# Performance work log

Measured on AMD Instinct MI355X. Metric: run time of the kernel, lower is better.

Reference implementation:

```python
import jax, jax.numpy as jnp
from jax import lax
import numpy as np

EPS = 1e-5
STRIDE = 4
K_NEIGHBORS = 16


def setup_inputs() -> dict:
    key = jax.random.key(0)
    ks = jax.random.split(key, 4)
    B, N, Cin, Cout = 16, 4096, 64, 128
    p1 = jax.random.normal(ks[0], (B, N, 3), dtype=jnp.float32)
    x1 = jax.random.normal(ks[1], (B, Cin, N), dtype=jnp.float32)
    w1 = jax.random.normal(ks[2], (Cout, Cin + 3), dtype=jnp.float32) * 0.05
    w2 = jax.random.normal(ks[3], (Cout, Cout), dtype=jnp.float32) * 0.05
    g1 = jnp.ones((Cout,), jnp.float32)
    b1 = jnp.zeros((Cout,), jnp.float32)
    g2 = jnp.ones((Cout,), jnp.float32)
    b2 = jnp.zeros((Cout,), jnp.float32)
    return {"p1": p1, "x1": x1, "w1": w1, "g1": g1, "b1": b1,
            "w2": w2, "g2": g2, "b2": b2}


def farthest_point_sampling(p, npoint):
    # p: [B, N, 3] -> centroids [B, npoint] (deterministic start at index 0)
    B, N, _ = p.shape
    gather_pt = jax.vmap(lambda pts, f: pts[f])  # [B,N,3],[B] -> [B,3]

    def step(carry, _):
        dist, farthest = carry
        centroid = gather_pt(p, farthest)                     # [B, 3]
        d = jnp.sum((p - centroid[:, None, :]) ** 2, -1)      # [B, N]
        dist = jnp.minimum(dist, d)
        new_far = jnp.argmax(dist, axis=-1).astype(jnp.int32)
        return (dist, new_far), farthest

    init = (jnp.full((B, N), 1e10, dtype=p.dtype), jnp.zeros((B,), jnp.int32))
    _, idxs = lax.scan(step, init, None, length=npoint)       # [npoint, B]
    return idxs.T                                             # [B, npoint]


def knn_point(k, xyz, new_xyz):
    # squared distances via gram trick; exclude all-zero points like the original
    n1 = jnp.sum(xyz ** 2, -1)                                # [B, N]
    n2 = jnp.sum(new_xyz ** 2, -1)                            # [B, M]
    d2 = n2[:, :, None] + n1[:, None, :] - 2.0 * jnp.einsum('bmc,bnc->bmn', new_xyz, xyz)
    zero_mask = jnp.all(xyz == 0, axis=-1)                    # [B, N]
    d2 = jnp.where(zero_mask[:, None, :], jnp.inf, d2)
    _, idx = lax.top_k(-d2, k)                                # smallest-k -> [B, M, k]
    return idx


def _bn_relu(h, g, b):
    # BatchNorm2d (training-mode batch stats, biased var) over (B, M, k) per channel
    m = jnp.mean(h, axis=(0, 1, 2), keepdims=True)
    v = jnp.mean((h - m) ** 2, axis=(0, 1, 2), keepdims=True)
    return jax.nn.relu(g * (h - m) * lax.rsqrt(v + EPS) + b)


def reference(p1, x1, w1, g1, b1, w2, g2, b2):
    B, N, _ = p1.shape
    M = max(1, N // STRIDE)
    k = K_NEIGHBORS

    idx = farthest_point_sampling(p1, M)                      # [B, M]
    gather2 = jax.vmap(lambda pts, i: pts[i])
    p2 = gather2(p1, idx)                                     # [B, M, 3]

    idx_knn = knn_point(k, p1, p2)                            # [B, M, k]
    grouped_p1 = gather2(p1, idx_knn)                         # [B, M, k, 3]
    xt = jnp.transpose(x1, (0, 2, 1))                         # [B, N, Cin]
    grouped_x1 = gather2(xt, idx_knn)                         # [B, M, k, Cin]

    rel = grouped_p1 - p2[:, :, None, :]                      # [B, M, k, 3]
    feats = jnp.concatenate([rel, grouped_x1], axis=-1)       # [B, M, k, 3+Cin]

    h = _bn_relu(jnp.einsum('bmkc,oc->bmko', feats, w1), g1, b1)
    h = _bn_relu(jnp.einsum('bmkc,oc->bmko', h, w2), g2, b2)
    new_features = jnp.max(h, axis=2)                         # maxpool over k -> [B, M, Cout]
    return p2, jnp.transpose(new_features, (0, 2, 1))         # ([B,M,3], [B,Cout,M])
```

## Files before the change

kernel.cpp:

```cpp
#include <hip/hip_runtime.h>
#include <hip/hip_bf16.h>
#include <hip/hip_cooperative_groups.h>
#include <cstdint>

namespace cg = cooperative_groups;

#define BB 16
#define NN 4096
#define MM 1024
#define KNB 16
#define CIN 64
#define COUT 128
#define RTOT (BB*MM*KNB)
#define AP1 104
#define AP2 136

typedef __attribute__((ext_vector_type(8))) short short8v;
typedef __attribute__((ext_vector_type(4))) float floatx4;
typedef __attribute__((ext_vector_type(2))) float f32x2;
typedef __attribute__((ext_vector_type(2))) unsigned int uint2v;

__device__ __forceinline__ float bflo(uint32_t u){ return __uint_as_float(u << 16); }
__device__ __forceinline__ float bfhi(uint32_t u){ return __uint_as_float(u & 0xffff0000u); }
__device__ __forceinline__ uint32_t f2bf_pk(float a, float b){
  uint32_t ua = __float_as_uint(a), ub = __float_as_uint(b);
  ua += 0x7fffu + ((ua >> 16) & 1u);
  ub += 0x7fffu + ((ub >> 16) & 1u);
  return (ua >> 16) | (ub & 0xffff0000u);
}
__device__ __forceinline__ uint16_t f2bf1(float a){
  uint32_t u = __float_as_uint(a);
  u += 0x7fffu + ((u >> 16) & 1u);
  return (uint16_t)(u >> 16);
}
template<int CTRL>
__device__ __forceinline__ float dpp_f(float v){
  return __int_as_float(__builtin_amdgcn_update_dpp(__float_as_int(v), __float_as_int(v), CTRL, 0xf, 0xf, false));
}
__device__ __forceinline__ float plmax16(float v){
#if __has_builtin(__builtin_amdgcn_permlane16_swap)
  uint2v r = __builtin_amdgcn_permlane16_swap(__float_as_uint(v), __float_as_uint(v), false, false);
  return fmaxf(__uint_as_float(r[0]), __uint_as_float(r[1]));
#else
  return fmaxf(v, __int_as_float(__builtin_amdgcn_ds_swizzle(__float_as_int(v), 0x401F)));
#endif
}
__device__ __forceinline__ float plmax32(float v){
#if __has_builtin(__builtin_amdgcn_permlane32_swap)
  uint2v r = __builtin_amdgcn_permlane32_swap(__float_as_uint(v), __float_as_uint(v), false, false);
  return fmaxf(__uint_as_float(r[0]), __uint_as_float(r[1]));
#else
  return fmaxf(v, __shfl_xor(v, 32));
#endif
}

struct FpsS { float4 pcv[NN]; float4 sel[MM]; unsigned long long candk[2][4]; };
struct TrS  { float t[64][65]; };
struct ConsS{ uint16_t Bh1[128*AP1]; uint16_t AhD[128*AP2];
              int winq[8*16]; float ssum[128]; float ssq[128]; };
union PreU  { FpsS fps; TrS tr; ConsS cons; };

__global__ __launch_bounds__(512, 2) void k_pre2(
    const float* __restrict__ p1, const float* __restrict__ x1,
    const float* __restrict__ w1,
    float* __restrict__ outp2, float* __restrict__ p2w,
    float4* __restrict__ p1n, uint16_t* __restrict__ xtb, float* __restrict__ Sz,
    uint16_t* __restrict__ h1, float* __restrict__ S1,
    int* __restrict__ prog, int* __restrict__ prep_done)
{
  __shared__ PreU u;
  const int blk = blockIdx.x, tid = threadIdx.x;
  const int lane = tid & 63, wid = tid >> 6;

  if (blk < 16){
    int b = blk;
    const float* pb = p1 + (size_t)b*NN*3;
    {
      float4 f[6];
      const float4* src = (const float4*)(pb + tid*24);
      #pragma unroll
      for (int j=0;j<6;j++) f[j] = src[j];
      const float* fa = (const float*)f;
      #pragma unroll
      for (int j=0;j<8;j++)
        u.fps.pcv[tid*8 + j] = make_float4(fa[3*j], fa[3*j+1], fa[3*j+2], 0.f);
    }
    __syncthreads();
    float4 c00 = u.fps.pcv[0];
    float cx = c00.x, cy = c00.y, cz = c00.z;
    if (tid==64) u.fps.sel[0] = make_float4(cx, cy, cz, 0.f);

    f32x2 px2[8] = {}, py2[8] = {}, pz2[8] = {}, ds2[8] = {};
    const int g0 = tid*16;
    if (wid < 4){
      #pragma unroll
      for (int j=0;j<8;j++){
        float4 a = u.fps.pcv[g0 + 2*j];
        float4 bq = u.fps.pcv[g0 + 2*j + 1];
        px2[j][0]=a.x; px2[j][1]=bq.x;
        py2[j][0]=a.y; py2[j][1]=bq.y;
        pz2[j][0]=a.z; pz2[j][1]=bq.z;
        ds2[j][0]=1e10f; ds2[j][1]=1e10f;
      }
    }

    for (int i=1;i<MM;i++){
      if (wid < 4){
        {
          #pragma clang fp contract(off)
          f32x2 cx2; cx2[0]=cx; cx2[1]=cx;
          f32x2 cy2; cy2[0]=cy; cy2[1]=cy;
          f32x2 cz2; cz2[0]=cz; cz2[1]=cz;
          #pragma unroll
          for (int j=0;j<8;j++){
            f32x2 dx = px2[j] - cx2;
            f32x2 dy = py2[j] - cy2;
            f32x2 dz = pz2[j] - cz2;
            f32x2 d  = dx*dx + dy*dy + dz*dz;
            ds2[j] = __builtin_elementwise_min(ds2[j], d);
          }
        }
        f32x2 t0 = __builtin_elementwise_max(ds2[0], ds2[1]);
        f32x2 t1 = __builtin_elementwise_max(ds2[2], ds2[3]);
        f32x2 t2 = __builtin_elementwise_max(ds2[4], ds2[5]);
        f32x2 t3 = __builtin_elementwise_max(ds2[6], ds2[7]);
        f32x2 u0 = __builtin_elementwise_max(t0, t1);
        f32x2 u1 = __builtin_elementwise_max(t2, t3);
        f32x2 vv = __builtin_elementwise_max(u0, u1);
        float lm = fmaxf(vv[0], vv[1]);
        int li = g0 + 15;
        #pragma unroll
        for (int j=14;j>=0;j--){
          float ev = ds2[j>>1][j & 1];
          li = (ev == lm) ? (g0 + j) : li;
        }
        float wm = lm;
        wm = fmaxf(wm, dpp_f<0xB1>(wm));
        wm = fmaxf(wm, dpp_f<0x4E>(wm));
        wm = fmaxf(wm, dpp_f<0x124>(wm));
        wm = fmaxf(wm, dpp_f<0x128>(wm));
        wm = plmax16(wm);
        wm = plmax32(wm);
        unsigned long long bmask = __ballot(lm == wm);
        int fl = __ffsll(bmask) - 1;
        int wi = __builtin_amdgcn_readlane(li, fl);
        if (lane == 0)
          u.fps.candk[i&1][wid] = (((unsigned long long)(unsigned)__float_as_uint(wm)) << 32)
                                   | (unsigned)(0xFFFFu ^ (unsigned)wi);
      }
      __syncthreads();
      if (wid < 4){
        const unsigned long long* cd = u.fps.candk[i&1];
        unsigned long long cq0=cd[0], cq1=cd[1], cq2=cd[2], cq3=cd[3];
        unsigned long long a0 = cq0>cq1?cq0:cq1, a1 = cq2>cq3?cq2:cq3;
        unsigned long long mb = a0>a1?a0:a1;
        int midx = (int)(0xFFFFu ^ (unsigned)(mb & 0xFFFFull));
        float4 cv = u.fps.pcv[midx];
        cx = cv.x; cy = cv.y; cz = cv.z;
        if (tid==64) u.fps.sel[i] = make_float4(cx, cy, cz, 0.f);
      } else if (wid == 4 && (i & 63) == 0){
        int e = i - 64 + lane;
        float4 s = u.fps.sel[e];
        float n2 = __fadd_rn(__fadd_rn(__fmul_rn(s.x,s.x),__fmul_rn(s.y,s.y)),__fmul_rn(s.z,s.z));
        *(float4*)(p2w + ((size_t)b*MM + e)*4) = make_float4(s.x, s.y, s.z, n2);
        if (lane == 0)
          __hip_atomic_store(&prog[b*16], i, __ATOMIC_RELEASE, __HIP_MEMORY_SCOPE_AGENT);
      }
    }
    __syncthreads();
    if (wid == 4){
      int e = 960 + lane;
      float4 s = u.fps.sel[e];
      float n2 = __fadd_rn(__fadd_rn(__fmul_rn(s.x,s.x),__fmul_rn(s.y,s.y)),__fmul_rn(s.z,s.z));
      *(float4*)(p2w + ((size_t)b*MM + e)*4) = make_float4(s.x, s.y, s.z, n2);
      if (lane == 0)
        __hip_atomic_store(&prog[b*16], MM, __ATOMIC_RELEASE, __HIP_MEMORY_SCOPE_AGENT);
    }
    for (int e = tid; e < MM; e += 512){
      float4 s = u.fps.sel[e];
      float* o = outp2 + ((size_t)b*MM + e)*3;
      o[0]=s.x; o[1]=s.y; o[2]=s.z;
    }
  } else {
    for (int i = (blk-16)*512 + tid; i < 16384; i += 240*512) Sz[i] = 0.f;
    for (int i = (blk-16)*512 + tid; i < BB*NN; i += 240*512){
      float x = p1[(size_t)i*3+0], y = p1[(size_t)i*3+1], z = p1[(size_t)i*3+2];
      float n = __fadd_rn(__fadd_rn(__fmul_rn(x,x),__fmul_rn(y,y)),__fmul_rn(z,z));
      p1n[i] = make_float4(x,y,z,n);
    }
    for (int tile = blk-16; tile < 1024; tile += 240){
      int b = tile >> 6, n0 = (tile & 63)*64;
      __syncthreads();
      int c = tid >> 3, q = tid & 7;
      const float* src = x1 + ((size_t)(b*64 + c))*NN + n0 + q*8;
      float4 f0 = *(const float4*)src, f1 = *(const float4*)(src+4);
      u.tr.t[c][q*8+0]=f0.x; u.tr.t[c][q*8+1]=f0.y; u.tr.t[c][q*8+2]=f0.z; u.tr.t[c][q*8+3]=f0.w;
      u.tr.t[c][q*8+4]=f1.x; u.tr.t[c][q*8+5]=f1.y; u.tr.t[c][q*8+6]=f1.z; u.tr.t[c][q*8+7]=f1.w;
      __syncthreads();
      int n = tid >> 3;
      uint32_t* dst = (uint32_t*)(xtb + ((size_t)(b*NN + n0 + n))*64 + q*8);
      #pragma unroll
      for (int j=0;j<4;j++)
        dst[j] = f2bf_pk(u.tr.t[q*8+2*j][n], u.tr.t[q*8+2*j+1][n]);
    }
    __threadfence();
    __syncthreads();
    if (tid == 0) atomicAdd(prep_done, 1);
    for (int e = tid; e < 128*96; e += 512){
      int o = e / 96, k = e - o*96;
      float v = (k < 64) ? w1[o*67 + 3 + k] : ((k < 67) ? w1[o*67 + (k-64)] : 0.f);
      u.cons.Bh1[o*AP1 + k] = f2bf1(v);
    }
    if (tid < 128){ u.cons.ssum[tid]=0.f; u.cons.ssq[tid]=0.f; }
    __syncthreads();
    {
      int pv = 0, sp = 0;
      if (lane == 0) pv = __hip_atomic_load(prep_done, __ATOMIC_ACQUIRE, __HIP_MEMORY_SCOPE_AGENT);
      pv = __shfl(pv, 0);
      while (pv < 240 && sp < (1<<16)){
        __builtin_amdgcn_s_sleep(64);
        if (lane == 0) pv = __hip_atomic_load(prep_done, __ATOMIC_ACQUIRE, __HIP_MEMORY_SCOPE_AGENT);
        pv = __shfl(pv, 0); sp++;
      }
    }
    int ml = lane & 15, quad = lane >> 4, seg = lane >> 4;
    int gw = (blk-16)*8 + wid;
    for (int qi = gw; qi < BB*MM; qi += 1920){
      int b = qi & 15, m = qi >> 4;
      int q2 = b*MM + m;
      {
        int pv = 0, sp = 0;
        if (lane == 0) pv = __hip_atomic_load(&prog[b*16], __ATOMIC_ACQUIRE, __HIP_MEMORY_SCOPE_AGENT);
        pv = __shfl(pv, 0);
        while (pv <= m && sp < (1<<16)){
          __builtin_amdgcn_s_sleep(64);
          if (lane == 0) pv = __hip_atomic_load(&prog[b*16], __ATOMIC_ACQUIRE, __HIP_MEMORY_SCOPE_AGENT);
          pv = __shfl(pv, 0); sp++;
        }
      }
      const float4 qv = *(const float4*)(p2w + (size_t)q2*4);
      const float4* pbn = p1n + (size_t)b*NN;
      float bd[16]; int bi[16];
      #pragma unroll
      for (int s=0;s<16;s++){ bd[s] = 1e30f; bi[s] = 0; }
      float wv = 1e30f; int wslot = 0;

      #define KPROC(T, PV) { \
        float dot = fmaf(qv.z, (PV).z, fmaf(qv.y, (PV).y, __fmul_rn(qv.x, (PV).x))); \
        float d2 = __fsub_rn(__fadd_rn(qv.w, (PV).w), __fmul_rn(2.0f, dot)); \
        if (d2 < wv){ \
          int c = (T)*64 + lane; \
          _Pragma("unroll") \
          for (int s=0;s<16;s++) if (s==wslot){ bd[s]=d2; bi[s]=c; } \
          wv = bd[0]; wslot = 0; \
          _Pragma("unroll") \
          for (int s=1;s<16;s++) if (bd[s] > wv){ wv = bd[s]; wslot = s; } \
        } }

      float4 cur = pbn[lane];
      for (int t=0;t<63;t++){
        float4 nx = pbn[(t+1)*64 + lane];
        KPROC(t, cur);
        cur = nx;
      }
      KPROC(63, cur);
      #undef KPROC

      float lv = bd[0]; int ls = 0;
      #pragma unroll
      for (int s=1;s<16;s++) if (bd[s] < lv){ lv = bd[s]; ls = s; }
      for (int r=0;r<16;r++){
        float rv = lv; int rl = lane;
        #pragma unroll
        for (int off=32; off>=1; off>>=1){
          float ov = __shfl_xor(rv, off); int ol = __shfl_xor(rl, off);
          if (ov < rv || (ov == rv && ol < rl)){ rv = ov; rl = ol; }
        }
        if (lane == rl){
          int idx = 0;
          #pragma unroll
          for (int s=0;s<16;s++) if (s==ls) idx = bi[s];
          u.cons.winq[wid*16 + r] = idx;
          #pragma unroll
          for (int s=0;s<16;s++) if (s==ls) bd[s] = 1e30f;
          lv = bd[0]; ls = 0;
          #pragma unroll
          for (int s=1;s<16;s++) if (bd[s] < lv){ lv = bd[s]; ls = s; }
        }
      }
      int n = u.cons.winq[wid*16 + ml];
      {
        const uint4* s4 = (const uint4*)(xtb + ((size_t)(b*NN + n))*64 + seg*16);
        uint4* d4 = (uint4*)(u.cons.AhD + (wid*16 + ml)*AP2 + seg*16);
        d4[0] = s4[0]; d4[1] = s4[1];
        if (seg == 0){
          const float* pp = p1 + ((size_t)(b*NN + n))*3;
          float rx = __fsub_rn(pp[0], qv.x);
          float ry = __fsub_rn(pp[1], qv.y);
          float rz = __fsub_rn(pp[2], qv.z);
          uint4* dr = (uint4*)(u.cons.AhD + (wid*16 + ml)*AP2 + 64);
          dr[0] = make_uint4(f2bf_pk(rx, ry), f2bf_pk(rz, 0.f), 0u, 0u);
          dr[1] = make_uint4(0u,0u,0u,0u);
          dr[2] = make_uint4(0u,0u,0u,0u);
          dr[3] = make_uint4(0u,0u,0u,0u);
        }
      }
      short8v af[3];
      #pragma unroll
      for (int kc=0;kc<3;kc++)
        af[kc] = *(const short8v*)(u.cons.AhD + (wid*16 + ml)*AP2 + kc*32 + quad*8);
      floatx4 acc[8];
      #pragma unroll
      for (int ct=0;ct<8;ct++) acc[ct] = (floatx4){0.f,0.f,0.f,0.f};
      #pragma unroll
      for (int ct=0;ct<8;ct++){
        #pragma unroll
        for (int kc=0;kc<3;kc++){
          short8v bf = *(const short8v*)(u.cons.Bh1 + (ct*16+ml)*AP1 + kc*32 + quad*8);
          acc[ct] = __builtin_amdgcn_mfma_f32_16x16x32_bf16(af[kc], bf, acc[ct], 0, 0, 0);
        }
      }
      float csum[8], csq[8];
      #pragma unroll
      for (int ct=0;ct<8;ct++){
        float a0=acc[ct][0], a1=acc[ct][1], a2=acc[ct][2], a3=acc[ct][3];
        float s = (a0+a1)+(a2+a3);
        float qq2 = (a0*a0+a1*a1)+(a2*a2+a3*a3);
        s += __shfl_xor(s,16);  s += __shfl_xor(s,32);
        qq2 += __shfl_xor(qq2,16); qq2 += __shfl_xor(qq2,32);
        csum[ct]=s; csq[ct]=qq2;
        #pragma unroll
        for (int r=0;r<4;r++)
          u.cons.AhD[(wid*16 + quad*4 + r)*AP2 + ct*16 + ml] = f2bf1(acc[ct][r]);
      }
      #pragma unroll
      for (int jj=0;jj<2;jj++){
        int ct = quad*2 + jj, col = ct*16 + ml;
        atomicAdd(&u.cons.ssum[col], csum[ct]);
        atomicAdd(&u.cons.ssq[col],  csq[ct]);
      }
      {
        const uint4* s4 = (const uint4*)(u.cons.AhD + (wid*16 + ml)*AP2 + seg*32);
        uint4* dst = (uint4*)(h1 + ((size_t)q2*16 + ml)*128 + seg*32);
        dst[0]=s4[0]; dst[1]=s4[1]; dst[2]=s4[2]; dst[3]=s4[3];
      }
    }
    __syncthreads();
    int cp = (blk & 31)*256;
    if (tid < 128){ atomicAdd(&S1[cp+tid], u.cons.ssum[tid]); atomicAdd(&S1[cp+128+tid], u.cons.ssq[tid]); }
  }
}

__global__ __launch_bounds__(256) void k_gemm2(const __hip_bfloat16* __restrict__ h1,
                                               const float* __restrict__ w2,
                                               const float* __restrict__ g1v, const float* __restrict__ b1v,
                                               const float* __restrict__ S1, float* __restrict__ S2,
                                               float* __restrict__ hmax, float* __restrict__ hmin){
  __shared__ __hip_bfloat16 Ah[64*AP2];
  __shared__ __hip_bfloat16 Bh[128*AP2];
  __shared__ float scb[128], shb[128], ssum[128], ssq[128];
  int tid = threadIdx.x;
  if (tid < 128){
    float s=0.f, q=0.f;
    for (int c=0;c<32;c++){ s += S1[c*256+tid]; q += S1[c*256+128+tid]; }
    float inv = 1.0f / (float)RTOT;
    float mean = s * inv;
    float var  = q * inv - mean*mean;
    float rs = 1.0f / sqrtf(var + 1e-5f);
    float scv = g1v[tid] * rs;
    scb[tid] = scv;
    shb[tid] = b1v[tid] - mean*scv;
    ssum[tid] = 0.f; ssq[tid] = 0.f;
  }
  {
    int o = tid >> 1, hf = tid & 1;
    const float4* wr = (const float4*)(w2 + (size_t)o*128 + hf*64);
    uint32_t* bd = (uint32_t*)(Bh + o*AP2 + hf*64);
    #pragma unroll
    for (int q=0;q<16;q++){
      float4 v = wr[q];
      bd[2*q]   = f2bf_pk(v.x, v.y);
      bd[2*q+1] = f2bf_pk(v.z, v.w);
    }
  }
  __syncthreads();
  int lane = tid & 63, wid = tid >> 6;
  int m0 = wid*16, ml = lane & 15, quad = lane >> 4;
  for (int j = 0; j < 4; j++){
    int tile = blockIdx.x*4 + j;
    int r0 = tile * 64;
    if (j) __syncthreads();
    {
      int row = tid >> 2, seg = tid & 3;
      const uint4* hp4 = (const uint4*)(h1 + ((size_t)(r0+row))*128 + seg*32);
      #pragma unroll
      for (int q=0;q<4;q++){
        uint4 u = hp4[q];
        int cg = seg*32 + q*8;
        uint32_t wv[4] = {u.x,u.y,u.z,u.w};
        uint32_t ov[4];
        #pragma unroll
        for (int t=0;t<4;t++){
          int c = cg + t*2;
          float a0 = fmaxf(fmaf(bflo(wv[t]), scb[c],   shb[c]),   0.f);
          float a1 = fmaxf(fmaf(bfhi(wv[t]), scb[c+1], shb[c+1]), 0.f);
          ov[t] = f2bf_pk(a0, a1);
        }
        *(uint4*)(Ah + row*AP2 + cg) = make_uint4(ov[0],ov[1],ov[2],ov[3]);
      }
    }
    __syncthreads();
    short8v af[4];
    #pragma unroll
    for (int kc=0;kc<4;kc++)
      af[kc] = *(const short8v*)(Ah + (m0+ml)*AP2 + kc*32 + quad*8);
    floatx4 acc[8];
    #pragma unroll
    for (int ct=0;ct<8;ct++) acc[ct] = (floatx4){0.f,0.f,0.f,0.f};
    #pragma unroll
    for (int ct=0;ct<8;ct++){
      #pragma unroll
      for (int kc=0;kc<4;kc++){
        short8v bf = *(const short8v*)(Bh + (ct*16+ml)*AP2 + kc*32 + quad*8);
        acc[ct] = __builtin_amdgcn_mfma_f32_16x16x32_bf16(af[kc], bf, acc[ct], 0, 0, 0);
      }
    }
    int mrow = (r0 >> 4) + wid;
    float cm[8], cn[8], cs[8], cq[8];
    #pragma unroll
    for (int ct=0;ct<8;ct++){
      float a0=acc[ct][0], a1=acc[ct][1], a2=acc[ct][2], a3=acc[ct][3];
      float mx = fmaxf(fmaxf(a0,a1), fmaxf(a2,a3));
      float mn = fminf(fminf(a0,a1), fminf(a2,a3));
      float s  = (a0+a1)+(a2+a3);
      float q2 = (a0*a0+a1*a1)+(a2*a2+a3*a3);
      mx = fmaxf(mx, __shfl_xor(mx,16)); mx = fmaxf(mx, __shfl_xor(mx,32));
      mn = fminf(mn, __shfl_xor(mn,16)); mn = fminf(mn, __shfl_xor(mn,32));
      s += __shfl_xor(s,16);  s += __shfl_xor(s,32);
      q2 += __shfl_xor(q2,16); q2 += __shfl_xor(q2,32);
      cm[ct]=mx; cn[ct]=mn; cs[ct]=s; cq[ct]=q2;
    }
    #pragma unroll
    for (int jj=0;jj<2;jj++){
      int ct = quad*2 + jj, col = ct*16 + ml;
      hmax[(size_t)mrow*128 + col] = cm[ct];
      hmin[(size_t)mrow*128 + col] = cn[ct];
      atomicAdd(&ssum[col], cs[ct]);
      atomicAdd(&ssq[col],  cq[ct]);
    }
  }
  __syncthreads();
  int cp = (blockIdx.x & 31)*256;
  if (tid < 128){ atomicAdd(&S2[cp+tid], ssum[tid]); atomicAdd(&S2[cp+128+tid], ssq[tid]); }
}

__global__ __launch_bounds__(256) void k_pool(const float* __restrict__ hmax, const float* __restrict__ hmin,
                                              const float* __restrict__ g2v, const float* __restrict__ b2v,
                                              const float* __restrict__ S2, float* __restrict__ out1){
  __shared__ float ot[128*65];
  __shared__ float scs[128], shs[128];
  int tid = threadIdx.x, blk = blockIdx.x;
  int b = blk >> 4, m0 = (blk & 15) * 64;
  if (tid < 128){
    float s=0.f, q=0.f;
    for (int c=0;c<32;c++){ s += S2[c*256+tid]; q += S2[c*256+128+tid]; }
    float inv = 1.0f / (float)RTOT;
    float mean = s * inv;
    float var  = q * inv - mean*mean;
    float rs = 1.0f / sqrtf(var + 1e-5f);
    float scv = g2v[tid] * rs;
    scs[tid] = scv;
    shs[tid] = b2v[tid] - mean*scv;
  }
  __syncthreads();
  int ml = tid >> 2, oq = tid & 3, o0 = oq*32;
  int gm = b*MM + m0 + ml;
  const float4* xr = (const float4*)(hmax + (size_t)gm*128 + o0);
  const float4* nr = (const float4*)(hmin + (size_t)gm*128 + o0);
  #pragma unroll
  for (int j2=0;j2<8;j2++){
    float4 hx = xr[j2], hn = nr[j2];
    float hv[4] = {hx.x, hx.y, hx.z, hx.w};
    float nv[4] = {hn.x, hn.y, hn.z, hn.w};
    #pragma unroll
    for (int e=0;e<4;e++){
      int c = o0 + j2*4 + e;
      float sc = scs[c], sh = shs[c];
      float h = (sc >= 0.f) ? hv[e] : nv[e];
      ot[c*65 + ml] = fmaxf(fmaf(h, sc, sh), 0.f);
    }
  }
  __syncthreads();
  int o = tid >> 1, mh = tid & 1;
  float* dst = out1 + ((size_t)(b*COUT + o))*MM + m0 + mh*32;
  #pragma unroll
  for (int j2=0;j2<8;j2++){
    float4 v;
    v.x=ot[o*65+mh*32+j2*4+0]; v.y=ot[o*65+mh*32+j2*4+1];
    v.z=ot[o*65+mh*32+j2*4+2]; v.w=ot[o*65+mh*32+j2*4+3];
    *(float4*)(dst + j2*4) = v;
  }
}

extern "C" void kernel_launch(void* const* d_in, const int* in_sizes, int n_in,
                              void* d_out, int out_size, void* d_ws, size_t ws_size,
                              hipStream_t stream) {
  (void)in_sizes; (void)n_in; (void)out_size; (void)ws_size;
  const float* p1 = (const float*)d_in[0];
  const float* x1 = (const float*)d_in[1];
  const float* w1 = (const float*)d_in[2];
  const float* g1 = (const float*)d_in[3];
  const float* b1 = (const float*)d_in[4];
  const float* w2 = (const float*)d_in[5];
  const float* g2 = (const float*)d_in[6];
  const float* b2 = (const float*)d_in[7];
  float* out = (float*)d_out;
  float* ws  = (float*)d_ws;

  uint16_t* xtb = (uint16_t*)ws;
  float4* p1n   = (float4*)(ws + 2097152);
  float*  p2w   = ws + 2621440;
  float*  S1    = ws + 2686976;
  float*  S2    = ws + 2695168;
  uint16_t* h1  = (uint16_t*)(ws + 2703872);
  float*  hmax  = ws + 19481088;
  float*  hmin  = ws + 21578240;
  int*    prog  = (int*)(ws + 23675392);
  int*    prep_done = (int*)(ws + 23675392) + 256;
  float*  outp2 = out;
  float*  out1  = out + 49152;

  hipMemsetAsync(prog, 0, 2048, stream);

  void* args[] = { (void*)&p1, (void*)&x1, (void*)&w1,
                   (void*)&outp2, (void*)&p2w,
                   (void*)&p1n, (void*)&xtb, (void*)&S1,
                   (void*)&h1, (void*)&S1, (void*)&prog, (void*)&prep_done };
  hipLaunchCooperativeKernel((void*)k_pre2, dim3(256), dim3(512), args, 0, stream);

  k_gemm2<<<1024, 256, 0, stream>>>((const __hip_bfloat16*)h1, w2, g1, b1, S1, S2, hmax, hmin);
  k_pool<<<256, 256, 0, stream>>>(hmax, hmin, g2, b2, S2, out1);
}
```

Measured before the change: 864.1 us.

## Replace per-iteration FPS block barrier with LDS spin-wait on tagged candidate keys

The per-iteration __syncthreads in the farthest-point-sampling loop is replaced by a flag scheme. Each of the four compute waves writes its candidate key, tagged with the iteration number, into a double-buffered LDS slot, then spins on relaxed atomic loads until all four tags match. Wave 4 now polls the tag with sleeps to publish p2 progress in chunks instead of joining every barrier, and the compute waves raise their scheduling priority. This is meant to cut barrier latency on the serial critical path. It risks relying on LDS visibility ordering without fences, and the spin loops have timeout escapes that could silently produce wrong results.

```diff
diff --git a/kernel.cpp b/kernel.cpp
--- a/kernel.cpp
+++ b/kernel.cpp
@@ -86,9 +86,10 @@
         u.fps.pcv[tid*8 + j] = make_float4(fa[3*j], fa[3*j+1], fa[3*j+2], 0.f);
     }
     __syncthreads();
+    if (tid < 8) u.fps.candk[tid>>2][tid&3] = 0ull;
     float4 c00 = u.fps.pcv[0];
     float cx = c00.x, cy = c00.y, cz = c00.z;
-    if (tid==64) u.fps.sel[0] = make_float4(cx, cy, cz, 0.f);
+    if (tid==0) u.fps.sel[0] = make_float4(cx, cy, cz, 0.f);
 
     f32x2 px2[8] = {}, py2[8] = {}, pz2[8] = {}, ds2[8] = {};
     const int g0 = tid*16;
@@ -103,9 +104,11 @@
         ds2[j][0]=1e10f; ds2[j][1]=1e10f;
       }
     }
-
-    for (int i=1;i<MM;i++){
-      if (wid < 4){
+    __syncthreads();
+
+    if (wid < 4){
+      __builtin_amdgcn_s_setprio(1);
+      for (int i=1;i<MM;i++){
         {
           #pragma clang fp contract(off)
           f32x2 cx2; cx2[0]=cx; cx2[1]=cx;
@@ -142,29 +145,48 @@
         wm = plmax16(wm);
         wm = plmax32(wm);
         unsigned long long bmask = __ballot(lm == wm);
-        int fl = __ffsll(bmask) - 1;
+        int fl = (int)__builtin_ctzll(bmask);
         int wi = __builtin_amdgcn_readlane(li, fl);
-        if (lane == 0)
-          u.fps.candk[i&1][wid] = (((unsigned long long)(unsigned)__float_as_uint(wm)) << 32)
-                                   | (unsigned)(0xFFFFu ^ (unsigned)wi);
-      }
-      __syncthreads();
-      if (wid < 4){
-        const unsigned long long* cd = u.fps.candk[i&1];
-        unsigned long long cq0=cd[0], cq1=cd[1], cq2=cd[2], cq3=cd[3];
-        unsigned long long a0 = cq0>cq1?cq0:cq1, a1 = cq2>cq3?cq2:cq3;
+        if (lane == 0){
+          unsigned long long key = (((unsigned long long)(unsigned)__float_as_uint(wm)) << 32)
+                                 | ((unsigned)i << 12) | (0xFFFu ^ (unsigned)wi);
+          u.fps.candk[i&1][wid] = key;
+        }
+        unsigned long long* cd = u.fps.candk[i&1];
+        unsigned long long k0,k1,k2,k3;
+        int sp = 0;
+        for (;;){
+          k0 = __hip_atomic_load(&cd[0], __ATOMIC_RELAXED, __HIP_MEMORY_SCOPE_WORKGROUP);
+          k1 = __hip_atomic_load(&cd[1], __ATOMIC_RELAXED, __HIP_MEMORY_SCOPE_WORKGROUP);
+          k2 = __hip_atomic_load(&cd[2], __ATOMIC_RELAXED, __HIP_MEMORY_SCOPE_WORKGROUP);
+          k3 = __hip_atomic_load(&cd[3], __ATOMIC_RELAXED, __HIP_MEMORY_SCOPE_WORKGROUP);
+          unsigned tg = ((unsigned)k0 >> 12) & ((unsigned)k1 >> 12)
+                      & ((unsigned)k2 >> 12) & ((unsigned)k3 >> 12);
+          if (tg == (unsigned)i || ++sp > (1<<22)) break;
+        }
+        unsigned long long a0 = k0>k1?k0:k1, a1 = k2>k3?k2:k3;
         unsigned long long mb = a0>a1?a0:a1;
-        int midx = (int)(0xFFFFu ^ (unsigned)(mb & 0xFFFFull));
+        int midx = (int)(0xFFFu ^ ((unsigned)mb & 0xFFFu));
         float4 cv = u.fps.pcv[midx];
         cx = cv.x; cy = cv.y; cz = cv.z;
-        if (tid==64) u.fps.sel[i] = make_float4(cx, cy, cz, 0.f);
-      } else if (wid == 4 && (i & 63) == 0){
-        int e = i - 64 + lane;
+        if (tid == 0) u.fps.sel[i] = make_float4(cx, cy, cz, 0.f);
+      }
+      __builtin_amdgcn_s_setprio(0);
+    } else if (wid == 4){
+      for (int t = 64; t <= 960; t += 64){
+        int sp = 0;
+        for (;;){
+          unsigned long long kk = __hip_atomic_load(&u.fps.candk[0][0],
+                                    __ATOMIC_RELAXED, __HIP_MEMORY_SCOPE_WORKGROUP);
+          if ((int)(((unsigned)kk) >> 12) >= t || ++sp > (1<<18)) break;
+          __builtin_amdgcn_s_sleep(32);
+        }
+        int e = t - 64 + lane;
         float4 s = u.fps.sel[e];
         float n2 = __fadd_rn(__fadd_rn(__fmul_rn(s.x,s.x),__fmul_rn(s.y,s.y)),__fmul_rn(s.z,s.z));
         *(float4*)(p2w + ((size_t)b*MM + e)*4) = make_float4(s.x, s.y, s.z, n2);
         if (lane == 0)
-          __hip_atomic_store(&prog[b*16], i, __ATOMIC_RELEASE, __HIP_MEMORY_SCOPE_AGENT);
+          __hip_atomic_store(&prog[b*16], t, __ATOMIC_RELEASE, __HIP_MEMORY_SCOPE_AGENT);
       }
     }
     __syncthreads();
```

Result: slower. 891.9 us (+3.2%).

## Fuse second GEMM and max-pool into one cooperative kernel with grid barrier

Applied to the files above, without the earlier changes.

Merges the second GEMM and the BN2/ReLU/max-pool stage into a single cooperative kernel of 256 blocks with 512 threads. Each block now covers one batch's 64 M-rows, keeps the per-row max and min in shared memory, and waits on an atomic counter until every block has contributed its BN2 statistics. The hmax/hmin global round trip and one kernel launch go away. In exchange the grid goes from 1024 small blocks to 256 larger ones that use more shared memory, plus a spin-wait barrier.

```diff
diff --git a/kernel.cpp b/kernel.cpp
--- a/kernel.cpp
+++ b/kernel.cpp
@@ -351,14 +351,18 @@
   }
 }
 
-__global__ __launch_bounds__(256) void k_gemm2(const __hip_bfloat16* __restrict__ h1,
-                                               const float* __restrict__ w2,
-                                               const float* __restrict__ g1v, const float* __restrict__ b1v,
-                                               const float* __restrict__ S1, float* __restrict__ S2,
-                                               float* __restrict__ hmax, float* __restrict__ hmin){
-  __shared__ __hip_bfloat16 Ah[64*AP2];
-  __shared__ __hip_bfloat16 Bh[128*AP2];
-  __shared__ float scb[128], shb[128], ssum[128], ssq[128];
+union GU { struct { __hip_bfloat16 Ah[64*AP2]; __hip_bfloat16 Bh[128*AP2]; } g;
+           float ot[128*65]; };
+__global__ __launch_bounds__(512) void k_gemm2p(const __hip_bfloat16* __restrict__ h1,
+                                                const float* __restrict__ w2,
+                                                const float* __restrict__ g1v, const float* __restrict__ b1v,
+                                                const float* __restrict__ S1, float* __restrict__ S2,
+                                                const float* __restrict__ g2v, const float* __restrict__ b2v,
+                                                float* __restrict__ out1, int* __restrict__ done2){
+  __shared__ GU su;
+  __shared__ float ex[64][128];
+  __shared__ float en[64][128];
+  __shared__ float scb[128], shb[128], ssumb[128], ssqb[128], scs[128], shs[128];
   int tid = threadIdx.x;
   if (tid < 128){
     float s=0.f, q=0.f;
@@ -370,14 +374,14 @@
     float scv = g1v[tid] * rs;
     scb[tid] = scv;
     shb[tid] = b1v[tid] - mean*scv;
-    ssum[tid] = 0.f; ssq[tid] = 0.f;
+    ssumb[tid] = 0.f; ssqb[tid] = 0.f;
   }
   {
-    int o = tid >> 1, hf = tid & 1;
-    const float4* wr = (const float4*)(w2 + (size_t)o*128 + hf*64);
-    uint32_t* bd = (uint32_t*)(Bh + o*AP2 + hf*64);
-    #pragma unroll
-    for (int q=0;q<16;q++){
+    int o = tid >> 2, q4 = tid & 3;
+    const float4* wr = (const float4*)(w2 + (size_t)o*128 + q4*32);
+    uint32_t* bd = (uint32_t*)(su.g.Bh + o*AP2 + q4*32);
+    #pragma unroll
+    for (int q=0;q<8;q++){
       float4 v = wr[q];
       bd[2*q]   = f2bf_pk(v.x, v.y);
       bd[2*q+1] = f2bf_pk(v.z, v.w);
@@ -385,19 +389,21 @@
   }
   __syncthreads();
   int lane = tid & 63, wid = tid >> 6;
-  int m0 = wid*16, ml = lane & 15, quad = lane >> 4;
-  for (int j = 0; j < 4; j++){
-    int tile = blockIdx.x*4 + j;
+  int wm0 = (wid >> 1) * 16;
+  int cth = (wid & 1) * 4;
+  int ml = lane & 15, quad = lane >> 4;
+  for (int j = 0; j < 16; j++){
+    int tile = blockIdx.x*16 + j;
     int r0 = tile * 64;
     if (j) __syncthreads();
     {
-      int row = tid >> 2, seg = tid & 3;
-      const uint4* hp4 = (const uint4*)(h1 + ((size_t)(r0+row))*128 + seg*32);
-      #pragma unroll
-      for (int q=0;q<4;q++){
-        uint4 u = hp4[q];
-        int cg = seg*32 + q*8;
-        uint32_t wv[4] = {u.x,u.y,u.z,u.w};
+      int row = tid >> 3, seg = tid & 7;
+      const uint4* hp4 = (const uint4*)(h1 + ((size_t)(r0+row))*128 + seg*16);
+      #pragma unroll
+      for (int q=0;q<2;q++){
+        uint4 uu = hp4[q];
+        int cg = seg*16 + q*8;
+        uint32_t wv[4] = {uu.x,uu.y,uu.z,uu.w};
         uint32_t ov[4];
         #pragma unroll
         for (int t=0;t<4;t++){
@@ -406,30 +412,30 @@
           float a1 = fmaxf(fmaf(bfhi(wv[t]), scb[c+1], shb[c+1]), 0.f);
           ov[t] = f2bf_pk(a0, a1);
         }
-        *(uint4*)(Ah + row*AP2 + cg) = make_uint4(ov[0],ov[1],ov[2],ov[3]);
+        *(uint4*)(su.g.Ah + row*AP2 + cg) = make_uint4(ov[0],ov[1],ov[2],ov[3]);
       }
     }
     __syncthreads();
     short8v af[4];
     #pragma unroll
     for (int kc=0;kc<4;kc++)
-      af[kc] = *(const short8v*)(Ah + (m0+ml)*AP2 + kc*32 + quad*8);
-    floatx4 acc[8];
-    #pragma unroll
-    for (int ct=0;ct<8;ct++) acc[ct] = (floatx4){0.f,0.f,0.f,0.f};
-    #pragma unroll
-    for (int ct=0;ct<8;ct++){
+      af[kc] = *(const short8v*)(su.g.Ah + (wm0+ml)*AP2 + kc*32 + quad*8);
+    floatx4 acc[4];
+    #pragma unroll
+    for (int c4=0;c4<4;c4++) acc[c4] = (floatx4){0.f,0.f,0.f,0.f};
+    #pragma unroll
+    for (int c4=0;c4<4;c4++){
       #pragma unroll
       for (int kc=0;kc<4;kc++){
-        short8v bf = *(const short8v*)(Bh + (ct*16+ml)*AP2 + kc*32 + quad*8);
-        acc[ct] = __builtin_amdgcn_mfma_f32_16x16x32_bf16(af[kc], bf, acc[ct], 0, 0, 0);
-      }
-    }
-    int mrow = (r0 >> 4) + wid;
-    float cm[8], cn[8], cs[8], cq[8];
-    #pragma unroll
-    for (int ct=0;ct<8;ct++){
-      float a0=acc[ct][0], a1=acc[ct][1], a2=acc[ct][2], a3=acc[ct][3];
+        short8v bf = *(const short8v*)(su.g.Bh + ((cth+c4)*16+ml)*AP2 + kc*32 + quad*8);
+        acc[c4] = __builtin_amdgcn_mfma_f32_16x16x32_bf16(af[kc], bf, acc[c4], 0, 0, 0);
+      }
+    }
+    int mloc = j*4 + (wid >> 1);
+    float cm[4], cn[4], cs[4], cq[4];
+    #pragma unroll
+    for (int c4=0;c4<4;c4++){
+      float a0=acc[c4][0], a1=acc[c4][1], a2=acc[c4][2], a3=acc[c4][3];
       float mx = fmaxf(fmaxf(a0,a1), fmaxf(a2,a3));
       float mn = fminf(fminf(a0,a1), fminf(a2,a3));
       float s  = (a0+a1)+(a2+a3);
@@ -438,29 +444,39 @@
       mn = fminf(mn, __shfl_xor(mn,16)); mn = fminf(mn, __shfl_xor(mn,32));
       s += __shfl_xor(s,16);  s += __shfl_xor(s,32);
       q2 += __shfl_xor(q2,16); q2 += __shfl_xor(q2,32);
-      cm[ct]=mx; cn[ct]=mn; cs[ct]=s; cq[ct]=q2;
-    }
-    #pragma unroll
-    for (int jj=0;jj<2;jj++){
-      int ct = quad*2 + jj, col = ct*16 + ml;
-      hmax[(size_t)mrow*128 + col] = cm[ct];
-      hmin[(size_t)mrow*128 + col] = cn[ct];
-      atomicAdd(&ssum[col], cs[ct]);
-      atomicAdd(&ssq[col],  cq[ct]);
+      cm[c4]=mx; cn[c4]=mn; cs[c4]=s; cq[c4]=q2;
+    }
+    {
+      float vmx = (quad==0)?cm[0]:((quad==1)?cm[1]:((quad==2)?cm[2]:cm[3]));
+      float vmn = (quad==0)?cn[0]:((quad==1)?cn[1]:((quad==2)?cn[2]:cn[3]));
+      float vs  = (quad==0)?cs[0]:((quad==1)?cs[1]:((quad==2)?cs[2]:cs[3]));
+      float vq  = (quad==0)?cq[0]:((quad==1)?cq[1]:((quad==2)?cq[2]:cq[3]));
+      int col = (cth + quad)*16 + ml;
+      ex[mloc][col] = vmx;
+      en[mloc][col] = vmn;
+      atomicAdd(&ssumb[col], vs);
+      atomicAdd(&ssqb[col],  vq);
     }
   }
   __syncthreads();
-  int cp = (blockIdx.x & 31)*256;
-  if (tid < 128){ atomicAdd(&S2[cp+tid], ssum[tid]); atomicAdd(&S2[cp+128+tid], ssq[tid]); }
-}
-
-__global__ __launch_bounds__(256) void k_pool(const float* __restrict__ hmax, const float* __restrict__ hmin,
-                                              const float* __restrict__ g2v, const float* __restrict__ b2v,
-                                              const float* __restrict__ S2, float* __restrict__ out1){
-  __shared__ float ot[128*65];
-  __shared__ float scs[128], shs[128];
-  int tid = threadIdx.x, blk = blockIdx.x;
-  int b = blk >> 4, m0 = (blk & 15) * 64;
+  {
+    int cp = (blockIdx.x & 31)*256;
+    if (tid < 128){ atomicAdd(&S2[cp+tid], ssumb[tid]); atomicAdd(&S2[cp+128+tid], ssqb[tid]); }
+  }
+  __threadfence();
+  __syncthreads();
+  if (tid == 0) __hip_atomic_fetch_add(done2, 1, __ATOMIC_ACQ_REL, __HIP_MEMORY_SCOPE_AGENT);
+  {
+    int dv = 0, sp = 0;
+    if (tid == 0){
+      do {
+        dv = __hip_atomic_load(done2, __ATOMIC_ACQUIRE, __HIP_MEMORY_SCOPE_AGENT);
+        if (dv >= 256) break;
+        __builtin_amdgcn_s_sleep(32);
+      } while (++sp < (1<<22));
+    }
+    __syncthreads();
+  }
   if (tid < 128){
     float s=0.f, q=0.f;
     for (int c=0;c<32;c++){ s += S2[c*256+tid]; q += S2[c*256+128+tid]; }
@@ -473,32 +489,30 @@
     shs[tid] = b2v[tid] - mean*scv;
   }
   __syncthreads();
-  int ml = tid >> 2, oq = tid & 3, o0 = oq*32;
-  int gm = b*MM + m0 + ml;
-  const float4* xr = (const float4*)(hmax + (size_t)gm*128 + o0);
-  const float4* nr = (const float4*)(hmin + (size_t)gm*128 + o0);
-  #pragma unroll
-  for (int j2=0;j2<8;j2++){
-    float4 hx = xr[j2], hn = nr[j2];
-    float hv[4] = {hx.x, hx.y, hx.z, hx.w};
-    float nv[4] = {hn.x, hn.y, hn.z, hn.w};
+  {
+    int m2 = tid >> 3, oq = tid & 7, o0 = oq*16;
+    #pragma unroll
+    for (int e=0;e<16;e++){
+      int c = o0 + e;
+      float sc = scs[c], sh = shs[c];
+      float h = (sc >= 0.f) ? ex[m2][c] : en[m2][c];
+      su.ot[c*65 + m2] = fmaxf(fmaf(h, sc, sh), 0.f);
+    }
+  }
+  __syncthreads();
+  {
+    int b = blockIdx.x >> 4, m0 = (blockIdx.x & 15)*64;
+    int o = tid >> 2, qr = tid & 3;
+    float* dst = out1 + ((size_t)(b*COUT + o))*MM + m0 + qr*16;
     #pragma unroll
     for (int e=0;e<4;e++){
-      int c = o0 + j2*4 + e;
-      float sc = scs[c], sh = shs[c];
-      float h = (sc >= 0.f) ? hv[e] : nv[e];
-      ot[c*65 + ml] = fmaxf(fmaf(h, sc, sh), 0.f);
-    }
-  }
-  __syncthreads();
-  int o = tid >> 1, mh = tid & 1;
-  float* dst = out1 + ((size_t)(b*COUT + o))*MM + m0 + mh*32;
-  #pragma unroll
-  for (int j2=0;j2<8;j2++){
-    float4 v;
-    v.x=ot[o*65+mh*32+j2*4+0]; v.y=ot[o*65+mh*32+j2*4+1];
-    v.z=ot[o*65+mh*32+j2*4+2]; v.w=ot[o*65+mh*32+j2*4+3];
-    *(float4*)(dst + j2*4) = v;
+      float4 v;
+      v.x = su.ot[o*65 + qr*16 + e*4 + 0];
+      v.y = su.ot[o*65 + qr*16 + e*4 + 1];
+      v.z = su.ot[o*65 + qr*16 + e*4 + 2];
+      v.w = su.ot[o*65 + qr*16 + e*4 + 3];
+      *(float4*)(dst + e*4) = v;
+    }
   }
 }
 
@@ -523,10 +537,9 @@
   float*  S1    = ws + 2686976;
   float*  S2    = ws + 2695168;
   uint16_t* h1  = (uint16_t*)(ws + 2703872);
-  float*  hmax  = ws + 19481088;
-  float*  hmin  = ws + 21578240;
   int*    prog  = (int*)(ws + 23675392);
   int*    prep_done = (int*)(ws + 23675392) + 256;
+  int*    done2 = (int*)(ws + 23675392) + 257;
   float*  outp2 = out;
   float*  out1  = out + 49152;
 
@@ -538,6 +551,9 @@
                    (void*)&h1, (void*)&S1, (void*)&prog, (void*)&prep_done };
   hipLaunchCooperativeKernel((void*)k_pre2, dim3(256), dim3(512), args, 0, stream);
 
-  k_gemm2<<<1024, 256, 0, stream>>>((const __hip_bfloat16*)h1, w2, g1, b1, S1, S2, hmax, hmin);
-  k_pool<<<256, 256, 0, stream>>>(hmax, hmin, g2, b2, S2, out1);
-}
+  const __hip_bfloat16* h1b = (const __hip_bfloat16*)h1;
+  void* args2[] = { (void*)&h1b, (void*)&w2, (void*)&g1, (void*)&b1,
+                    (void*)&S1, (void*)&S2, (void*)&g2, (void*)&b2,
+                    (void*)&out1, (void*)&done2 };
+  hipLaunchCooperativeKernel((void*)k_gemm2p, dim3(256), dim3(512), args2, 0, stream);
+}
```

After: 937.0 us. 1.08x slower.
